# Performance work log

Hardware: AMD Instinct MI355X
Metric: run time of the kernel (lower is better)

## Reference

```python
import jax, jax.numpy as jnp
import numpy as np

B, T, M, D = 4, 512, 16, 128
P, H = 128, 4
E = P // H


def _glorot(k, shape, fan_in, fan_out):
    lim = np.sqrt(6.0 / (fan_in + fan_out)).astype(np.float32)
    return jax.random.uniform(k, shape, jnp.float32, -lim, lim)


def setup_inputs() -> dict:
    key = jax.random.key(0)
    ks = jax.random.split(key, 12)
    inp = jax.random.normal(ks[0], (B, T, M, D), jnp.float32)
    pos = jax.random.normal(ks[1], (B, T, 1, D), jnp.float32)
    # padding mask: valid time steps per batch element (ensures no fully-masked softmax row)
    lengths = jax.random.randint(ks[2], (B,), T // 2, T + 1)
    mask = jnp.broadcast_to(jnp.arange(T)[None, :, None] < lengths[:, None, None], (B, T, M))
    Wq = _glorot(ks[3], (M, P, D), D, P)
    Wk = _glorot(ks[4], (M, P, D), D, P)
    Wv = _glorot(ks[5], (M, P, D), D, P)
    Wq_t = _glorot(ks[6], (M, P, D), D, P)
    Wk_t = _glorot(ks[7], (M, P, D), D, P)
    Bq = jnp.zeros((M, P), jnp.float32)
    Bk = jnp.zeros((M, P), jnp.float32)
    Bv = jnp.zeros((M, P), jnp.float32)
    Bq_t = jnp.zeros((M, P), jnp.float32)
    Bk_t = jnp.zeros((M, P), jnp.float32)
    return {"inp": inp, "pos": pos, "mask": mask,
            "Wq": Wq, "Bq": Bq, "Wk": Wk, "Bk": Bk, "Wv": Wv, "Bv": Bv,
            "Wq_t": Wq_t, "Bq_t": Bq_t, "Wk_t": Wk_t, "Bk_t": Bk_t}


def reference(inp, pos, mask, Wq, Bq, Wk, Bk, Wv, Bv, Wq_t, Bq_t, Wk_t, Bk_t):
    b, t, m, d = inp.shape
    p = Wq.shape[1]
    h, e = H, P // H
    # per-modality projections: (m,p,d) x (b,t,m,d) -> (b,t,m,p)
    q = jnp.einsum('mpd,btmd->btmp', Wq, inp) + Bq
    k = jnp.einsum('mpd,btmd->btmp', Wk, inp) + Bk
    v = jnp.einsum('mpd,btmd->btmp', Wv, inp) + Bv
    pos0 = pos[:, :, 0, :]  # (b,t,d); broadcasts across m
    q_t = jnp.einsum('mpd,btd->btmp', Wq_t, pos0) + Bq_t
    k_t = jnp.einsum('mpd,btd->btmp', Wk_t, pos0) + Bk_t

    def split_heads(x):  # (b,t,m,p) -> (b,m,h,t,e)
        return x.reshape(b, t, m, h, e).transpose(0, 2, 3, 1, 4)

    q, k, v, q_t, k_t = map(split_heads, (q, k, v, q_t, k_t))
    # dual bilinear score: content + positional
    score = (jnp.einsum('bmhte,bmhse->bmhts', q, k)
             + jnp.einsum('bmhte,bmhse->bmhts', q_t, k_t)) / (2.0 * np.sqrt(e).astype(np.float32))
    causal = jnp.tril(jnp.ones((t, t), bool))  # (t,t)
    score = jnp.where(causal, score, -jnp.inf)
    km = mask.transpose(0, 2, 1)[:, :, None, None, :]  # (b,m,1,1,t)
    score = jnp.where(km, score, -jnp.inf)
    w = jax.nn.softmax(score, axis=-1)
    w = jnp.where(km, w, 0.0)
    w = jnp.where(causal, w, 0.0)
    # dropout is identity at inference (drop_rate ignored)
    out = jnp.einsum('bmhts,bmhse->bmhte', w, v)
    return out.transpose(0, 3, 1, 2, 4).reshape(b, t, m, p)
```

## Files before the change

### kernel.cpp

```cpp
#include <hip/hip_runtime.h>

#define Bn 4
#define Tn 512
#define Mn 16
#define Dn 128
#define Pn 128
#define Hn 4
#define SCALE 0.08838834764831845f

typedef unsigned short u16;
typedef unsigned int u32;
typedef short s16;
typedef __attribute__((ext_vector_type(8))) s16 bf16x8;
typedef __attribute__((ext_vector_type(4))) float f32x4;

#define NWE (Mn * Pn * Dn)

__device__ __forceinline__ u16 f2b(float f) {
  u32 x; __builtin_memcpy(&x, &f, 4);
  x += 0x7fffu + ((x >> 16) & 1u);
  return (u16)(x >> 16);
}
__device__ __forceinline__ u32 pack2(float a, float b) {
  return (u32)f2b(a) | ((u32)f2b(b) << 16);
}
__device__ __forceinline__ bf16x8 ld8(const u16* p) {
  bf16x8 r; __builtin_memcpy(&r, p, 16); return r;
}
__device__ __forceinline__ f32x4 mfma16(bf16x8 a, bf16x8 b, f32x4 c) {
  return __builtin_amdgcn_mfma_f32_16x16x32_bf16(a, b, c, 0, 0, 0);
}

__global__ __launch_bounds__(256) void prep(
    const void* __restrict__ mask, const float* __restrict__ inp,
    const float* __restrict__ pos, const float* __restrict__ Wq,
    const float* __restrict__ Wk, const float* __restrict__ Wv,
    const float* __restrict__ Wqt, const float* __restrict__ Wkt,
    int* __restrict__ lens, u16* __restrict__ Xb, u16* __restrict__ Pb,
    u16* __restrict__ Wb) {
  if (blockIdx.x < Bn) {
    const int b = blockIdx.x;
    __shared__ int cnt[256];
    const u32 w0 = ((const u32*)mask)[0];
    const int mode = (w0 == 1u) ? 0 : (w0 == 0x3F800000u) ? 1
                   : (w0 == 0x3F803F80u) ? 2 : 3;
    int c = 0;
    for (int t = threadIdx.x; t < Tn; t += 256) {
      const size_t idx = ((size_t)b * Tn + t) * Mn;
      int nz;
      if (mode == 0)      nz = (((const int*)mask)[idx] != 0);
      else if (mode == 1) nz = (((const u32*)mask)[idx] != 0u);
      else if (mode == 2) nz = (((const u16*)mask)[idx] != 0);
      else                nz = (((const unsigned char*)mask)[idx] != 0);
      c += nz;
    }
    cnt[threadIdx.x] = c;
    __syncthreads();
    for (int s = 128; s > 0; s >>= 1) {
      if (threadIdx.x < (unsigned)s) cnt[threadIdx.x] += cnt[threadIdx.x + s];
      __syncthreads();
    }
    if (threadIdx.x == 0) lens[b] = cnt[0];
  }

  const int NI8 = Bn * Tn * Mn * Dn / 8;
  const int NP8 = Bn * Tn * Dn / 8;
  const int NW8 = NWE / 8;
  const int total = NI8 + NP8 + 5 * NW8;
  for (int u = blockIdx.x * 256 + threadIdx.x; u < total; u += gridDim.x * 256) {
    const float* s; u16* d; int off;
    if (u < NI8) { s = inp; d = Xb; off = u; }
    else if (u < NI8 + NP8) { s = pos; d = Pb; off = u - NI8; }
    else {
      const int r = u - NI8 - NP8;
      const int w = r >> 15; off = r & (NW8 - 1);
      switch (w) {
        case 0:  s = Wq;  d = Wb;            break;
        case 1:  s = Wk;  d = Wb + NWE;      break;
        case 2:  s = Wv;  d = Wb + 2 * NWE;  break;
        case 3:  s = Wqt; d = Wb + 3 * NWE;  break;
        default: s = Wkt; d = Wb + 4 * NWE;  break;
      }
    }
    const float4 a0 = *(const float4*)(s + (size_t)off * 8);
    const float4 a1 = *(const float4*)(s + (size_t)off * 8 + 4);
    uint4 dd;
    dd.x = pack2(a0.x, a0.y); dd.y = pack2(a0.z, a0.w);
    dd.z = pack2(a1.x, a1.y); dd.w = pack2(a1.z, a1.w);
    *(uint4*)(d + (size_t)off * 8) = dd;
  }
}

__global__ __launch_bounds__(256) void proj_mfma(
    const u16* __restrict__ Xb, const u16* __restrict__ Pb,
    const u16* __restrict__ Wb,
    const float* __restrict__ Bq, const float* __restrict__ Bk,
    const float* __restrict__ Bv, const float* __restrict__ Bqt,
    const float* __restrict__ Bkt,
    u16* __restrict__ Qa, u16* __restrict__ Ka, u16* __restrict__ Qb,
    u16* __restrict__ Kb, u16* __restrict__ Vt) {
  const int tid = threadIdx.x;
  const int bid = blockIdx.x;
  const int tsel = bid % 5;
  const int m = (bid / 5) % Mn;
  const int rt0 = (bid / (5 * Mn)) * 128;

  const float* Bb; int usepos, doscale; u16* dst;
  switch (tsel) {
    case 0:  Bb = Bq;  usepos = 0; doscale = 1; dst = Qa; break;
    case 1:  Bb = Bk;  usepos = 0; doscale = 0; dst = Ka; break;
    case 2:  Bb = Bv;  usepos = 0; doscale = 0; dst = Vt; break;
    case 3:  Bb = Bqt; usepos = 1; doscale = 1; dst = Qb; break;
    default: Bb = Bkt; usepos = 1; doscale = 0; dst = Kb; break;
  }
  const u16* A = usepos ? Pb : Xb;
  const u16* Wsrc = Wb + (size_t)tsel * NWE + (size_t)m * Pn * Dn;

  __shared__ __align__(16) u16 Xs[128 * 72];
  __shared__ __align__(16) u16 Ws2[128 * 72];

  const int wv = tid >> 6, lane = tid & 63;
  const int quad = lane >> 4, l16 = lane & 15;

  f32x4 acc[2][8];
#pragma unroll
  for (int i = 0; i < 2; ++i)
#pragma unroll
    for (int n = 0; n < 8; ++n) acc[i][n] = (f32x4){0.f, 0.f, 0.f, 0.f};

  const u16* Als = (tsel == 2) ? Xs : Ws2;
  const u16* Bls = (tsel == 2) ? Ws2 : Xs;

  for (int kh = 0; kh < 2; ++kh) {
    bf16x8 xr[4], wr[4];
#pragma unroll
    for (int it = 0; it < 4; ++it) {
      const int c = tid + it * 256;
      const int row = c >> 3, c8 = (c & 7) * 8, col = kh * 64 + c8;
      const size_t sx = usepos ? ((size_t)(rt0 + row) * Dn + col)
                               : (((size_t)(rt0 + row) * Mn + m) * Dn + col);
      xr[it] = ld8(A + sx);
    }
#pragma unroll
    for (int it = 0; it < 4; ++it) {
      const int c = tid + it * 256;
      const int row = c >> 3, c8 = (c & 7) * 8, col = kh * 64 + c8;
      wr[it] = ld8(Wsrc + (size_t)row * Dn + col);
    }
    if (kh) __syncthreads();
#pragma unroll
    for (int it = 0; it < 4; ++it) {
      const int c = tid + it * 256;
      const int row = c >> 3, c8 = (c & 7) * 8;
      *(bf16x8*)&Xs[row * 72 + c8] = xr[it];
    }
#pragma unroll
    for (int it = 0; it < 4; ++it) {
      const int c = tid + it * 256;
      const int row = c >> 3, c8 = (c & 7) * 8;
      *(bf16x8*)&Ws2[row * 72 + c8] = wr[it];
    }
    __syncthreads();
#pragma unroll
    for (int kc = 0; kc < 2; ++kc) {
      const int ko = kc * 32 + quad * 8;
      const bf16x8 a0 = ld8(&Als[(wv * 32 + l16) * 72 + ko]);
      const bf16x8 a1 = ld8(&Als[(wv * 32 + 16 + l16) * 72 + ko]);
#pragma unroll
      for (int n = 0; n < 8; ++n) {
        const bf16x8 bn = ld8(&Bls[(n * 16 + l16) * 72 + ko]);
        acc[0][n] = mfma16(a0, bn, acc[0][n]);
        acc[1][n] = mfma16(a1, bn, acc[1][n]);
      }
    }
    if (kh == 0) __syncthreads();
  }

  const int b = rt0 >> 9;
  const int tb = rt0 & (Tn - 1);

  if (tsel == 2) {
    const int tl0 = tb + wv * 32;
#pragma unroll
    for (int n = 0; n < 8; ++n) {
      const int h = n >> 1, e = (n & 1) * 16 + l16;
      const float bias = Bb[m * Pn + n * 16 + l16];
      const int bmh = (b * Mn + m) * Hn + h;
      const size_t rowv = ((size_t)bmh * 32 + e) * Tn;
#pragma unroll
      for (int qs = 0; qs < 2; ++qs) {
        const int t0 = tl0 + qs * 16 + quad * 4;
        uint2 d;
        d.x = pack2(acc[qs][n][0] + bias, acc[qs][n][1] + bias);
        d.y = pack2(acc[qs][n][2] + bias, acc[qs][n][3] + bias);
        *(uint2*)&dst[rowv + t0] = d;
      }
    }
  } else {
    const int bmh = (b * Mn + m) * Hn + wv;
#pragma unroll
    for (int pf = 0; pf < 2; ++pf) {
      const int p0 = wv * 32 + pf * 16 + quad * 4;
      const float4 b4 = *(const float4*)&Bb[m * Pn + p0];
#pragma unroll
      for (int tf = 0; tf < 8; ++tf) {
        const int t = tb + tf * 16 + l16;
        float v0 = acc[pf][tf][0] + b4.x;
        float v1 = acc[pf][tf][1] + b4.y;
        float v2 = acc[pf][tf][2] + b4.z;
        float v3 = acc[pf][tf][3] + b4.w;
        if (doscale) { v0 *= SCALE; v1 *= SCALE; v2 *= SCALE; v3 *= SCALE; }
        uint2 d; d.x = pack2(v0, v1); d.y = pack2(v2, v3);
        *(uint2*)&dst[((size_t)bmh * Tn + t) * 32 + pf * 16 + quad * 4] = d;
      }
    }
  }
}

__global__ __launch_bounds__(128, 4) void attn_flash(
    const u16* __restrict__ Qa, const u16* __restrict__ Ka,
    const u16* __restrict__ Qb, const u16* __restrict__ Kb,
    const u16* __restrict__ Vt, const int* __restrict__ lens,
    float* __restrict__ out) {
  __shared__ __align__(16) u16 Ps[2 * 32 * 72];

  const int tid = threadIdx.x;
  const int wv = tid >> 6, lane = tid & 63;
  const int quad = lane >> 4, l16 = lane & 15;

  const int wu = blockIdx.x * 2 + wv;
  const int pair = wu & 7;
  const int bmh = wu >> 3;
  const int b = bmh >> 6;
  const int len = lens[b];

  const size_t rowbase = (size_t)bmh * Tn;
  const size_t vbase = (size_t)bmh * 32 * Tn;
  u16* myPs = &Ps[wv * 32 * 72];
  const int mm = (bmh >> 2) & (Mn - 1);
  const int h = bmh & (Hn - 1);

#pragma unroll 1
  for (int half = 0; half < 2; ++half) {
    const int qt = half ? (15 - pair) : pair;
    const int q0 = qt * 32;

    bf16x8 qf[2][2];
#pragma unroll
    for (int qs = 0; qs < 2; ++qs) {
      const size_t r = (rowbase + q0 + qs * 16 + l16) * 32 + quad * 8;
      qf[qs][0] = ld8(Qa + r);
      qf[qs][1] = ld8(Qb + r);
    }

    f32x4 O[2][2];
#pragma unroll
    for (int qs = 0; qs < 2; ++qs)
#pragma unroll
      for (int es = 0; es < 2; ++es) O[qs][es] = (f32x4){0.f, 0.f, 0.f, 0.f};
    float mrow[2] = {-1e30f, -1e30f}, lsum[2] = {0.f, 0.f};

    const int s_hi = min(q0 + 32, len);
    for (int s0 = 0; s0 < s_hi; s0 += 64) {
      f32x4 S[2][4];
#pragma unroll
      for (int st = 0; st < 4; ++st) {
        const size_t kr = (rowbase + s0 + st * 16 + l16) * 32 + quad * 8;
        const bf16x8 k0 = ld8(Ka + kr);
        const bf16x8 k1 = ld8(Kb + kr);
#pragma unroll
        for (int qs = 0; qs < 2; ++qs)
          S[qs][st] = mfma16(k1, qf[qs][1],
                             mfma16(k0, qf[qs][0], (f32x4){0.f, 0.f, 0.f, 0.f}));
      }

#pragma unroll
      for (int qs = 0; qs < 2; ++qs) {
        const int q = q0 + qs * 16 + l16;
        const int qcap = min(q, len - 1);
        const int sb = s0 + quad * 4;
        float cmax = -1e30f;
#pragma unroll
        for (int st = 0; st < 4; ++st)
#pragma unroll
          for (int reg = 0; reg < 4; ++reg) {
            const int s = sb + st * 16 + reg;
            const float v = (s <= qcap) ? S[qs][st][reg] : -1e30f;
            S[qs][st][reg] = v;
            cmax = fmaxf(cmax, v);
          }
        cmax = fmaxf(cmax, __shfl_xor(cmax, 16));
        cmax = fmaxf(cmax, __shfl_xor(cmax, 32));
        const float mnew = fmaxf(mrow[qs], cmax);
        const float alpha = __expf(mrow[qs] - mnew);
        mrow[qs] = mnew;
        float rsum = 0.f;
        u32 pk[4][2];
#pragma unroll
        for (int st = 0; st < 4; ++st) {
          const float p0 = __expf(S[qs][st][0] - mnew);
          const float p1 = __expf(S[qs][st][1] - mnew);
          const float p2 = __expf(S[qs][st][2] - mnew);
          const float p3 = __expf(S[qs][st][3] - mnew);
          rsum += (p0 + p1) + (p2 + p3);
          pk[st][0] = pack2(p0, p1);
          pk[st][1] = pack2(p2, p3);
        }
        rsum += __shfl_xor(rsum, 16);
        rsum += __shfl_xor(rsum, 32);
        lsum[qs] = lsum[qs] * alpha + rsum;
#pragma unroll
        for (int es = 0; es < 2; ++es)
#pragma unroll
          for (int reg = 0; reg < 4; ++reg) O[qs][es][reg] *= alpha;
#pragma unroll
        for (int st = 0; st < 4; ++st) {
          uint2 d; d.x = pk[st][0]; d.y = pk[st][1];
          *(uint2*)&myPs[(qs * 16 + l16) * 72 + st * 16 + quad * 4] = d;
        }
      }

#pragma unroll
      for (int kc = 0; kc < 2; ++kc) {
        const int ko = kc * 32 + quad * 8;
        const bf16x8 pf0 = ld8(&myPs[l16 * 72 + ko]);
        const bf16x8 pf1 = ld8(&myPs[(16 + l16) * 72 + ko]);
        const bf16x8 vf0 = ld8(Vt + vbase + (size_t)l16 * Tn + s0 + ko);
        const bf16x8 vf1 = ld8(Vt + vbase + (size_t)(16 + l16) * Tn + s0 + ko);
        O[0][0] = mfma16(vf0, pf0, O[0][0]);
        O[0][1] = mfma16(vf1, pf0, O[0][1]);
        O[1][0] = mfma16(vf0, pf1, O[1][0]);
        O[1][1] = mfma16(vf1, pf1, O[1][1]);
      }
    }

#pragma unroll
    for (int qs = 0; qs < 2; ++qs) {
      const float linv = 1.0f / lsum[qs];
      const int t = q0 + qs * 16 + l16;
      const size_t ob = (((size_t)b * Tn + t) * Mn + mm) * Pn + h * 32 + quad * 4;
#pragma unroll
      for (int es = 0; es < 2; ++es) {
        float4 o;
        o.x = O[qs][es][0] * linv; o.y = O[qs][es][1] * linv;
        o.z = O[qs][es][2] * linv; o.w = O[qs][es][3] * linv;
        *(float4*)&out[ob + es * 16] = o;
      }
    }
  }
}

extern "C" void kernel_launch(void* const* d_in, const int* in_sizes, int n_in,
                              void* d_out, int out_size, void* d_ws, size_t ws_size,
                              hipStream_t stream) {
  const float* inp = (const float*)d_in[0];
  const float* pos = (const float*)d_in[1];
  const void* mask = d_in[2];
  const float* Wq  = (const float*)d_in[3];
  const float* Bq  = (const float*)d_in[4];
  const float* Wk  = (const float*)d_in[5];
  const float* Bk  = (const float*)d_in[6];
  const float* Wv  = (const float*)d_in[7];
  const float* Bv  = (const float*)d_in[8];
  const float* Wqt = (const float*)d_in[9];
  const float* Bqt = (const float*)d_in[10];
  const float* Wkt = (const float*)d_in[11];
  const float* Bkt = (const float*)d_in[12];
  float* out = (float*)d_out;

  const size_t nA = (size_t)Bn * Mn * Hn * Tn * 32;
  u16* Qa = (u16*)d_ws;
  u16* Ka = Qa + nA;
  u16* Qb = Ka + nA;
  u16* Kb = Qb + nA;
  u16* Vt = Kb + nA;
  int* lens = (int*)(Vt + nA);
  u16* Xb = (u16*)(lens + 8);
  u16* Pb = Xb + (size_t)Bn * Tn * Mn * Dn;
  u16* Wb = Pb + (size_t)Bn * Tn * Dn;

  prep<<<1024, 256, 0, stream>>>(mask, inp, pos, Wq, Wk, Wv, Wqt, Wkt,
                                 lens, Xb, Pb, Wb);
  proj_mfma<<<(Bn * Tn / 128) * Mn * 5, 256, 0, stream>>>(
      Xb, Pb, Wb, Bq, Bk, Bv, Bqt, Bkt, Qa, Ka, Qb, Kb, Vt);
  attn_flash<<<(Bn * Mn * Hn * 8) / 2, 128, 0, stream>>>(
      Qa, Ka, Qb, Kb, Vt, lens, out);
}
```

Baseline: 147.7 us.

## Fuse paired query tiles in one pass sharing K/V loads with double-buffered K

Each wave now processes its two balanced query tiles (pair and 15-pair) together in a single loop over key blocks, so each K and V tile is loaded once and used for both, instead of being reloaded in two sequential passes. K fragments are double-buffered in registers so the next block's load is issued before the current block's compute. s_setprio is raised around the MFMA sections, and the block-to-work mapping is changed so the blocks sharing a head are spread across the grid. The price is higher register pressure: launch bounds drop from 4 to 2 blocks per CU and the LDS footprint doubles, which may reduce occupancy and latency hiding.

```diff
diff --git a/kernel.cpp b/kernel.cpp
--- a/kernel.cpp
+++ b/kernel.cpp
@@ -217,123 +217,169 @@
   }
 }
 
-__global__ __launch_bounds__(128, 4) void attn_flash(
+__global__ __launch_bounds__(128, 2) void attn_flash(
     const u16* __restrict__ Qa, const u16* __restrict__ Ka,
     const u16* __restrict__ Qb, const u16* __restrict__ Kb,
     const u16* __restrict__ Vt, const int* __restrict__ lens,
     float* __restrict__ out) {
-  __shared__ __align__(16) u16 Ps[2 * 32 * 72];
+  __shared__ __align__(16) u16 Ps[2 * 2 * 32 * 72];
 
   const int tid = threadIdx.x;
   const int wv = tid >> 6, lane = tid & 63;
   const int quad = lane >> 4, l16 = lane & 15;
 
-  const int wu = blockIdx.x * 2 + wv;
-  const int pair = wu & 7;
-  const int bmh = wu >> 3;
+  const int blk = blockIdx.x;
+  const int bmh = blk & 255;
+  const int pair = ((blk >> 8) << 1) + wv;
   const int b = bmh >> 6;
   const int len = lens[b];
 
+  const int qtA = pair, qtB = 15 - pair;
+  const int q0A = qtA * 32, q0B = qtB * 32;
   const size_t rowbase = (size_t)bmh * Tn;
   const size_t vbase = (size_t)bmh * 32 * Tn;
-  u16* myPs = &Ps[wv * 32 * 72];
+  u16* PsA = &Ps[(wv * 2 + 0) * 32 * 72];
+  u16* PsB = &Ps[(wv * 2 + 1) * 32 * 72];
   const int mm = (bmh >> 2) & (Mn - 1);
   const int h = bmh & (Hn - 1);
 
-#pragma unroll 1
-  for (int half = 0; half < 2; ++half) {
-    const int qt = half ? (15 - pair) : pair;
-    const int q0 = qt * 32;
-
-    bf16x8 qf[2][2];
+  const int sA = min(q0A + 32, len), sB = min(q0B + 32, len);
+  const int nA = (sA + 63) >> 6, nB = (sB + 63) >> 6;
+
+  auto loadK = [&](bf16x8 (&kr)[8], int s0) {
+#pragma unroll
+    for (int st = 0; st < 4; ++st) {
+      const size_t kr0 = (rowbase + s0 + st * 16 + l16) * 32 + quad * 8;
+      kr[st * 2]     = ld8(Ka + kr0);
+      kr[st * 2 + 1] = ld8(Kb + kr0);
+    }
+  };
+  auto loadV = [&](bf16x8 (&vf)[4], int s0) {
+    const int ko0 = quad * 8, ko1 = 32 + quad * 8;
+    vf[0] = ld8(Vt + vbase + (size_t)l16 * Tn + s0 + ko0);
+    vf[1] = ld8(Vt + vbase + (size_t)(16 + l16) * Tn + s0 + ko0);
+    vf[2] = ld8(Vt + vbase + (size_t)l16 * Tn + s0 + ko1);
+    vf[3] = ld8(Vt + vbase + (size_t)(16 + l16) * Tn + s0 + ko1);
+  };
+
+  bf16x8 kR0[8], kR1[8];
+  loadK(kR0, 0);
+
+  bf16x8 qfA[2][2], qfB[2][2];
+#pragma unroll
+  for (int qs = 0; qs < 2; ++qs) {
+    const size_t rA = (rowbase + q0A + qs * 16 + l16) * 32 + quad * 8;
+    qfA[qs][0] = ld8(Qa + rA); qfA[qs][1] = ld8(Qb + rA);
+    const size_t rB = (rowbase + q0B + qs * 16 + l16) * 32 + quad * 8;
+    qfB[qs][0] = ld8(Qa + rB); qfB[qs][1] = ld8(Qb + rB);
+  }
+
+  f32x4 OA[2][2], OB[2][2];
+#pragma unroll
+  for (int qs = 0; qs < 2; ++qs)
+#pragma unroll
+    for (int es = 0; es < 2; ++es) {
+      OA[qs][es] = (f32x4){0.f, 0.f, 0.f, 0.f};
+      OB[qs][es] = (f32x4){0.f, 0.f, 0.f, 0.f};
+    }
+  float mA[2] = {-1e30f, -1e30f}, lA[2] = {0.f, 0.f};
+  float mB[2] = {-1e30f, -1e30f}, lB[2] = {0.f, 0.f};
+
+  auto doTile = [&](const bf16x8 (&kc)[8], const bf16x8 (&qf)[2][2],
+                    f32x4 (&O)[2][2], float (&mrow)[2], float (&lsum)[2],
+                    u16* myPs, int q0, int s0, const bf16x8 (&vf)[4]) {
+    f32x4 S[2][4];
+    __builtin_amdgcn_s_setprio(1);
+#pragma unroll
+    for (int st = 0; st < 4; ++st)
+#pragma unroll
+      for (int qs = 0; qs < 2; ++qs)
+        S[qs][st] = mfma16(kc[st * 2 + 1], qf[qs][1],
+                           mfma16(kc[st * 2], qf[qs][0],
+                                  (f32x4){0.f, 0.f, 0.f, 0.f}));
+    __builtin_amdgcn_s_setprio(0);
 #pragma unroll
     for (int qs = 0; qs < 2; ++qs) {
-      const size_t r = (rowbase + q0 + qs * 16 + l16) * 32 + quad * 8;
-      qf[qs][0] = ld8(Qa + r);
-      qf[qs][1] = ld8(Qb + r);
-    }
-
-    f32x4 O[2][2];
-#pragma unroll
-    for (int qs = 0; qs < 2; ++qs)
-#pragma unroll
-      for (int es = 0; es < 2; ++es) O[qs][es] = (f32x4){0.f, 0.f, 0.f, 0.f};
-    float mrow[2] = {-1e30f, -1e30f}, lsum[2] = {0.f, 0.f};
-
-    const int s_hi = min(q0 + 32, len);
-    for (int s0 = 0; s0 < s_hi; s0 += 64) {
-      f32x4 S[2][4];
+      const int q = q0 + qs * 16 + l16;
+      const int qcap = min(q, len - 1);
+      const int sb = s0 + quad * 4;
+      float cmax = -1e30f;
+#pragma unroll
+      for (int st = 0; st < 4; ++st)
+#pragma unroll
+        for (int reg = 0; reg < 4; ++reg) {
+          const int s = sb + st * 16 + reg;
+          const float v = (s <= qcap) ? S[qs][st][reg] : -1e30f;
+          S[qs][st][reg] = v;
+          cmax = fmaxf(cmax, v);
+        }
+      cmax = fmaxf(cmax, __shfl_xor(cmax, 16));
+      cmax = fmaxf(cmax, __shfl_xor(cmax, 32));
+      const float mnew = fmaxf(mrow[qs], cmax);
+      const float alpha = __expf(mrow[qs] - mnew);
+      mrow[qs] = mnew;
+      float rsum = 0.f;
+      u32 pk[4][2];
 #pragma unroll
       for (int st = 0; st < 4; ++st) {
-        const size_t kr = (rowbase + s0 + st * 16 + l16) * 32 + quad * 8;
-        const bf16x8 k0 = ld8(Ka + kr);
-        const bf16x8 k1 = ld8(Kb + kr);
-#pragma unroll
-        for (int qs = 0; qs < 2; ++qs)
-          S[qs][st] = mfma16(k1, qf[qs][1],
-                             mfma16(k0, qf[qs][0], (f32x4){0.f, 0.f, 0.f, 0.f}));
-      }
-
-#pragma unroll
-      for (int qs = 0; qs < 2; ++qs) {
-        const int q = q0 + qs * 16 + l16;
-        const int qcap = min(q, len - 1);
-        const int sb = s0 + quad * 4;
-        float cmax = -1e30f;
-#pragma unroll
-        for (int st = 0; st < 4; ++st)
-#pragma unroll
-          for (int reg = 0; reg < 4; ++reg) {
-            const int s = sb + st * 16 + reg;
-            const float v = (s <= qcap) ? S[qs][st][reg] : -1e30f;
-            S[qs][st][reg] = v;
-            cmax = fmaxf(cmax, v);
-          }
-        cmax = fmaxf(cmax, __shfl_xor(cmax, 16));
-        cmax = fmaxf(cmax, __shfl_xor(cmax, 32));
-        const float mnew = fmaxf(mrow[qs], cmax);
-        const float alpha = __expf(mrow[qs] - mnew);
-        mrow[qs] = mnew;
-        float rsum = 0.f;
-        u32 pk[4][2];
-#pragma unroll
-        for (int st = 0; st < 4; ++st) {
-          const float p0 = __expf(S[qs][st][0] - mnew);
-          const float p1 = __expf(S[qs][st][1] - mnew);
-          const float p2 = __expf(S[qs][st][2] - mnew);
-          const float p3 = __expf(S[qs][st][3] - mnew);
-          rsum += (p0 + p1) + (p2 + p3);
-          pk[st][0] = pack2(p0, p1);
-          pk[st][1] = pack2(p2, p3);
-        }
-        rsum += __shfl_xor(rsum, 16);
-        rsum += __shfl_xor(rsum, 32);
-        lsum[qs] = lsum[qs] * alpha + rsum;
-#pragma unroll
-        for (int es = 0; es < 2; ++es)
-#pragma unroll
-          for (int reg = 0; reg < 4; ++reg) O[qs][es][reg] *= alpha;
-#pragma unroll
-        for (int st = 0; st < 4; ++st) {
-          uint2 d; d.x = pk[st][0]; d.y = pk[st][1];
-          *(uint2*)&myPs[(qs * 16 + l16) * 72 + st * 16 + quad * 4] = d;
-        }
-      }
-
-#pragma unroll
-      for (int kc = 0; kc < 2; ++kc) {
-        const int ko = kc * 32 + quad * 8;
-        const bf16x8 pf0 = ld8(&myPs[l16 * 72 + ko]);
-        const bf16x8 pf1 = ld8(&myPs[(16 + l16) * 72 + ko]);
-        const bf16x8 vf0 = ld8(Vt + vbase + (size_t)l16 * Tn + s0 + ko);
-        const bf16x8 vf1 = ld8(Vt + vbase + (size_t)(16 + l16) * Tn + s0 + ko);
-        O[0][0] = mfma16(vf0, pf0, O[0][0]);
-        O[0][1] = mfma16(vf1, pf0, O[0][1]);
-        O[1][0] = mfma16(vf0, pf1, O[1][0]);
-        O[1][1] = mfma16(vf1, pf1, O[1][1]);
-      }
-    }
-
+        const float p0 = __expf(S[qs][st][0] - mnew);
+        const float p1 = __expf(S[qs][st][1] - mnew);
+        const float p2 = __expf(S[qs][st][2] - mnew);
+        const float p3 = __expf(S[qs][st][3] - mnew);
+        rsum += (p0 + p1) + (p2 + p3);
+        pk[st][0] = pack2(p0, p1);
+        pk[st][1] = pack2(p2, p3);
+      }
+      rsum += __shfl_xor(rsum, 16);
+      rsum += __shfl_xor(rsum, 32);
+      lsum[qs] = lsum[qs] * alpha + rsum;
+#pragma unroll
+      for (int es = 0; es < 2; ++es)
+#pragma unroll
+        for (int reg = 0; reg < 4; ++reg) O[qs][es][reg] *= alpha;
+#pragma unroll
+      for (int st = 0; st < 4; ++st) {
+        uint2 d; d.x = pk[st][0]; d.y = pk[st][1];
+        *(uint2*)&myPs[(qs * 16 + l16) * 72 + st * 16 + quad * 4] = d;
+      }
+    }
+    __builtin_amdgcn_s_setprio(1);
+#pragma unroll
+    for (int kc2 = 0; kc2 < 2; ++kc2) {
+      const int ko = kc2 * 32 + quad * 8;
+      const bf16x8 pf0 = ld8(&myPs[l16 * 72 + ko]);
+      const bf16x8 pf1 = ld8(&myPs[(16 + l16) * 72 + ko]);
+      O[0][0] = mfma16(vf[kc2 * 2], pf0, O[0][0]);
+      O[0][1] = mfma16(vf[kc2 * 2 + 1], pf0, O[0][1]);
+      O[1][0] = mfma16(vf[kc2 * 2], pf1, O[1][0]);
+      O[1][1] = mfma16(vf[kc2 * 2 + 1], pf1, O[1][1]);
+    }
+    __builtin_amdgcn_s_setprio(0);
+  };
+
+  int ci = 0;
+  while (true) {
+    {
+      const int s0 = ci << 6;
+      bf16x8 vf[4];
+      loadV(vf, s0);
+      if (ci + 1 < nB) loadK(kR1, (ci + 1) << 6);
+      if (ci < nA) doTile(kR0, qfA, OA, mA, lA, PsA, q0A, s0, vf);
+      doTile(kR0, qfB, OB, mB, lB, PsB, q0B, s0, vf);
+      if (++ci == nB) break;
+    }
+    {
+      const int s0 = ci << 6;
+      bf16x8 vf[4];
+      loadV(vf, s0);
+      if (ci + 1 < nB) loadK(kR0, (ci + 1) << 6);
+      if (ci < nA) doTile(kR1, qfA, OA, mA, lA, PsA, q0A, s0, vf);
+      doTile(kR1, qfB, OB, mB, lB, PsB, q0B, s0, vf);
+      if (++ci == nB) break;
+    }
+  }
+
+  auto epi = [&](const f32x4 (&O)[2][2], const float (&lsum)[2], int q0) {
 #pragma unroll
     for (int qs = 0; qs < 2; ++qs) {
       const float linv = 1.0f / lsum[qs];
@@ -347,7 +393,9 @@
         *(float4*)&out[ob + es * 16] = o;
       }
     }
-  }
+  };
+  epi(OA, lA, q0A);
+  epi(OB, lB, q0B);
 }
 
 extern "C" void kernel_launch(void* const* d_in, const int* in_sizes, int n_in,
@@ -383,6 +431,6 @@
                                  lens, Xb, Pb, Wb);
   proj_mfma<<<(Bn * Tn / 128) * Mn * 5, 256, 0, stream>>>(
       Xb, Pb, Wb, Bq, Bk, Bv, Bqt, Bkt, Qa, Ka, Qb, Kb, Vt);
-  attn_flash<<<(Bn * Mn * Hn * 8) / 2, 128, 0, stream>>>(
+  attn_flash<<<Bn * Mn * Hn * 4, 128, 0, stream>>>(
       Qa, Ka, Qb, Kb, Vt, lens, out);
 }
```

After: 148.4 us. No clear change (+0.5%).
